# Kernel tuning notes

Measured on AMD Instinct MI355X. Metric: run time of the kernel, lower is better.

## Reference

```python
import math
import jax, jax.numpy as jnp
import numpy as np

E_DIM = 256
R_DIM = 256
HID = 512
B = 1024
H = 200
LN_EPS = 1e-5


def layer_norm(x, g, b):
    mu = jnp.mean(x, axis=-1, keepdims=True)
    var = jnp.mean((x - mu) ** 2, axis=-1, keepdims=True)
    return (x - mu) * jax.lax.rsqrt(var + LN_EPS) * g + b


def setup_inputs() -> dict:
    key = jax.random.key(0)
    ks = jax.random.split(key, 16)
    s = lambda fan: 1.0 / math.sqrt(fan)
    inp = {
        "e_emb": jax.random.normal(ks[0], (B, E_DIM), jnp.float32),
        "hist_ent_emb": jax.random.normal(ks[1], (B, H, E_DIM), jnp.float32),
        "hist_rel_emb": jax.random.normal(ks[2], (B, H, R_DIM), jnp.float32),
        "hist_time_raw": jax.random.randint(ks[3], (B, H), 0, 1000, jnp.int32),
        "query_time": jax.random.randint(ks[4], (B,), 0, 1000, jnp.int32),
        "hist_mask": jax.random.bernoulli(ks[5], 0.8, (B, H)),
        # parameters
        "W_rel": jax.random.uniform(ks[6], (E_DIM, R_DIM), jnp.float32, -s(R_DIM), s(R_DIM)),
        "W_q": jax.random.uniform(ks[7], (E_DIM, E_DIM), jnp.float32, -s(E_DIM), s(E_DIM)),
        "log_gamma": jnp.asarray(-3.0, jnp.float32),
        "W1": jax.random.uniform(ks[8], (2 * E_DIM, 4 * E_DIM), jnp.float32, -s(4 * E_DIM), s(4 * E_DIM)),
        "b1": jnp.zeros((2 * E_DIM,), jnp.float32),
        "ln1_g": jnp.ones((2 * E_DIM,), jnp.float32),
        "ln1_b": jnp.zeros((2 * E_DIM,), jnp.float32),
        "W2": jax.random.uniform(ks[9], (E_DIM, 2 * E_DIM), jnp.float32, -s(2 * E_DIM), s(2 * E_DIM)),
        "b2": jnp.zeros((E_DIM,), jnp.float32),
        "ln2_g": jnp.ones((E_DIM,), jnp.float32),
        "ln2_b": jnp.zeros((E_DIM,), jnp.float32),
        "Wc": jax.random.uniform(ks[10], (HID, E_DIM), jnp.float32, -s(E_DIM), s(E_DIM)),
        "bc": jnp.zeros((HID,), jnp.float32),
        "lnc_g": jnp.ones((HID,), jnp.float32),
        "lnc_b": jnp.zeros((HID,), jnp.float32),
    }
    return inp


def reference(e_emb, hist_ent_emb, hist_rel_emb, hist_time_raw, query_time, hist_mask,
              W_rel, W_q, log_gamma, W1, b1, ln1_g, ln1_b, W2, b2, ln2_g, ln2_b,
              Wc, bc, lnc_g, lnc_b):
    E = e_emb.shape[-1]
    # DistMult messages: (B,H,E)
    rel_projected = jnp.einsum("bhr,er->bhe", hist_rel_emb, W_rel)
    messages = hist_ent_emb * rel_projected
    # time decay
    time_diff = jnp.maximum(query_time.astype(jnp.float32)[:, None] - hist_time_raw.astype(jnp.float32), 0.0)
    decay = jnp.exp(-jnp.exp(log_gamma) * time_diff)  # (B,H)
    messages_dec = messages * decay[..., None]
    # query-conditioned attention
    q_repr = e_emb @ W_q.T  # (B,E)
    attn_raw = jnp.einsum("be,bhe->bh", q_repr, messages_dec) / math.sqrt(E)
    attn_raw = jnp.where(hist_mask, attn_raw, -1e9)
    attn = jax.nn.softmax(attn_raw, axis=-1)
    # PNA aggregation over valid neighbors
    valid_f = hist_mask.astype(jnp.float32)[..., None]  # (B,H,1)
    n_valid = jnp.maximum(jnp.sum(valid_f, axis=1), 1.0)  # (B,1)
    valid_msgs = messages * valid_f
    mean_msg = jnp.sum(valid_msgs, axis=1) / n_valid
    max_msg = jnp.max(valid_msgs, axis=1)
    attn_msg = jnp.einsum("bh,bhe->be", attn, messages)
    combined = jnp.concatenate([mean_msg, max_msg, attn_msg, e_emb], axis=-1)  # (B,4E)
    # out_proj MLP (dropout = identity, eval mode)
    h1 = jax.nn.gelu(layer_norm(combined @ W1.T + b1, ln1_g, ln1_b), approximate=False)
    dynamic_emb = layer_norm(h1 @ W2.T + b2, ln2_g, ln2_b)  # (B,E)
    ctx = jax.nn.gelu(layer_norm(dynamic_emb @ Wc.T + bc, lnc_g, lnc_b), approximate=False)  # (B,HID)
    return dynamic_emb, ctx
```

## Files before the change

kernel.cpp:

```cpp
#include <hip/hip_runtime.h>
#include <hip/hip_bf16.h>
#include <math.h>

#define B_SZ 1024
#define H_SZ 200
#define E_SZ 256
#define R_SZ 256
#define LN_EPS 1e-5f
#define NEG_HUGE -3.0e38f

typedef short bf16x8 __attribute__((ext_vector_type(8)));
typedef float f32x4 __attribute__((ext_vector_type(4)));

static __device__ inline short f2bf(float f) {
  union { float f; unsigned int u; } v; v.f = f;
  unsigned int u = v.u;
  unsigned int r = (u + 0x7fffu + ((u >> 16) & 1u)) >> 16;
  return (short)(unsigned short)r;
}

static __device__ inline float mask_at(const void* m, size_t idx, int is_b8) {
  if (is_b8) return ((const unsigned char*)m)[idx] ? 1.f : 0.f;
  return ((const int*)m)[idx] ? 1.f : 0.f;
}

__global__ void detect_mask_kernel(const unsigned char* __restrict__ mask,
                                   int* __restrict__ flag) {
  __shared__ int cnt;
  if (threadIdx.x == 0) cnt = 0;
  __syncthreads();
  int c = 0;
  for (int i = threadIdx.x; i < 4096; i += 256) c += mask[i] ? 1 : 0;
  atomicAdd(&cnt, c);
  __syncthreads();
  if (threadIdx.x == 0) *flag = (cnt > 2048) ? 1 : 0;
}

__global__ __launch_bounds__(256) void qrepr_kernel(
    const float* __restrict__ e_emb, const float* __restrict__ Wq,
    float* __restrict__ q_out) {
  __shared__ float emb[4][E_SZ];
  const int t = threadIdx.x;
  const int b0 = blockIdx.x * 4;
  for (int r = 0; r < 4; ++r) emb[r][t] = e_emb[(size_t)(b0 + r) * E_SZ + t];
  __syncthreads();
  float acc[4] = {0.f, 0.f, 0.f, 0.f};
  const float4* wrow = (const float4*)(Wq + (size_t)t * E_SZ);
  for (int k4 = 0; k4 < E_SZ / 4; ++k4) {
    float4 w = wrow[k4];
    const int k = k4 * 4;
#pragma unroll
    for (int r = 0; r < 4; ++r)
      acc[r] += emb[r][k] * w.x + emb[r][k + 1] * w.y + emb[r][k + 2] * w.z +
                emb[r][k + 3] * w.w;
  }
  for (int r = 0; r < 4; ++r) q_out[(size_t)(b0 + r) * E_SZ + t] = acc[r];
}

#define AGG_LDS_BYTES 152576

__global__ __launch_bounds__(512, 2) void agg_kernel(
    const float* __restrict__ rel, const float* __restrict__ ent,
    const int* __restrict__ htime, const int* __restrict__ qtime,
    const void* __restrict__ mask, const int* __restrict__ mflag,
    const float* __restrict__ Wrel, const float* __restrict__ qws,
    const float* __restrict__ e_emb, const float* __restrict__ log_gamma,
    float* __restrict__ comb) {
  extern __shared__ char smem[];
  short* Wsw = (short*)smem;
  short* Asw = (short*)(smem + 131072);
  float* q_s = (float*)(smem + 147456);
  float* attn_acc = (float*)(smem + 148480);
  float* mean_b = (float*)(smem + 149504);
  float* max_b = (float*)(smem + 150528);
  float* s_part = (float*)(smem + 151552);
  float* decay_s = (float*)(smem + 152064);
  float* maskf_s = (float*)(smem + 152192);
  float* p_s = (float*)(smem + 152320);
  float* scal = (float*)(smem + 152448);

  const int t = threadIdx.x;
  const int lane = t & 63;
  const int w = t >> 6;
  const int rh = w >> 2;
  const int cg = w & 3;
  const int q4 = lane >> 4;
  const int cl = lane & 15;
  const float gamma = expf(log_gamma[0]);
  const int is_b8 = *mflag;

  for (int pass = 0; pass < 16; ++pass) {
    const int idx = pass * 512 + t;
    const int e = idx >> 5;
    const int rc = idx & 31;
    const float4* src = (const float4*)(Wrel + (size_t)e * R_SZ + rc * 8);
    float4 a0 = src[0], a1 = src[1];
    const int ks = rc >> 2;
    const int lidx = ((rc & 3) << 4) | (e & 15);
    const int csub = e >> 4;
    bf16x8 v;
    v[0] = f2bf(a0.x); v[1] = f2bf(a0.y); v[2] = f2bf(a0.z); v[3] = f2bf(a0.w);
    v[4] = f2bf(a1.x); v[5] = f2bf(a1.y); v[6] = f2bf(a1.z); v[7] = f2bf(a1.w);
    *(bf16x8*)(Wsw + (((csub * 8 + ks) * 64 + lidx) << 3)) = v;
  }

  for (int bi = 0; bi < 4; ++bi) {
    const int b = blockIdx.x + 256 * bi;
    if (t < 256) { attn_acc[t] = 0.f; q_s[t] = qws[(size_t)b * E_SZ + t]; }
    if (t == 0) { scal[0] = NEG_HUGE; scal[1] = 0.f; scal[2] = 0.f; scal[3] = 0.f; }
    float mean4[4] = {0.f, 0.f, 0.f, 0.f};
    float max4[4] = {NEG_HUGE, NEG_HUGE, NEG_HUGE, NEG_HUGE};
    const float qtf = (float)qtime[b];
    __syncthreads();

    for (int tile = 0; tile < 7; ++tile) {
      const int h0 = tile * 32;
      {
        const int row = t >> 4;
        const int rcc = t & 15;
        const int h = h0 + row;
        bf16x8 v0 = {}; bf16x8 v1 = {};
        if (h < H_SZ) {
          const float4* src =
              (const float4*)(rel + ((size_t)b * H_SZ + h) * R_SZ + rcc * 16);
          float4 a0 = src[0], a1 = src[1], a2 = src[2], a3 = src[3];
          v0[0] = f2bf(a0.x); v0[1] = f2bf(a0.y); v0[2] = f2bf(a0.z); v0[3] = f2bf(a0.w);
          v0[4] = f2bf(a1.x); v0[5] = f2bf(a1.y); v0[6] = f2bf(a1.z); v0[7] = f2bf(a1.w);
          v1[0] = f2bf(a2.x); v1[1] = f2bf(a2.y); v1[2] = f2bf(a2.z); v1[3] = f2bf(a2.w);
          v1[4] = f2bf(a3.x); v1[5] = f2bf(a3.y); v1[6] = f2bf(a3.z); v1[7] = f2bf(a3.w);
        }
        const int rh2 = row >> 4, rlow = row & 15;
        const int rr0 = rcc * 2, rr1 = rcc * 2 + 1;
        *(bf16x8*)(Asw + (((rh2 * 8 + (rr0 >> 2)) * 64 + (((rr0 & 3) << 4) | rlow)) << 3)) = v0;
        *(bf16x8*)(Asw + (((rh2 * 8 + (rr1 >> 2)) * 64 + (((rr1 & 3) << 4) | rlow)) << 3)) = v1;
      }
      if (t < 32) {
        const int h = h0 + t;
        float mf = 0.f, dc = 0.f;
        if (h < H_SZ) {
          mf = mask_at(mask, (size_t)b * H_SZ + h, is_b8);
          float td = fmaxf(qtf - (float)htime[(size_t)b * H_SZ + h], 0.f);
          dc = expf(-gamma * td);
        }
        maskf_s[t] = mf; decay_s[t] = dc;
      }
      __syncthreads();

      f32x4 acc[4] = {};
      for (int ks = 0; ks < 8; ++ks) {
        bf16x8 av = *(bf16x8*)(Asw + (((rh * 8 + ks) * 64 + lane) << 3));
#pragma unroll
        for (int sub = 0; sub < 4; ++sub) {
          bf16x8 bv = *(bf16x8*)(Wsw + ((((cg * 4 + sub) * 8 + ks) * 64 + lane) << 3));
          acc[sub] = __builtin_amdgcn_mfma_f32_16x16x32_bf16(av, bv, acc[sub], 0, 0, 0);
        }
      }

      float msgv[16];
      float sc[4];
#pragma unroll
      for (int reg = 0; reg < 4; ++reg) {
        const int row = rh * 16 + q4 * 4 + reg;
        const int h = h0 + row;
        const float mf = maskf_s[row];
        const bool realrow = (h < H_SZ);
        float srow = 0.f;
#pragma unroll
        for (int sub = 0; sub < 4; ++sub) {
          const int e = cg * 64 + sub * 16 + cl;
          float entv = realrow ? ent[((size_t)b * H_SZ + h) * E_SZ + e] : 0.f;
          float m = acc[sub][reg] * entv;
          msgv[reg * 4 + sub] = m;
          mean4[sub] += mf * m;
          float cand = realrow ? (mf != 0.f ? m : 0.f) : NEG_HUGE;
          max4[sub] = fmaxf(max4[sub], cand);
          srow += q_s[e] * m;
        }
        sc[reg] = srow;
      }
#pragma unroll
      for (int m = 1; m <= 8; m <<= 1)
#pragma unroll
        for (int reg = 0; reg < 4; ++reg) sc[reg] += __shfl_xor(sc[reg], m, 64);
      if (cl == 0)
#pragma unroll
        for (int reg = 0; reg < 4; ++reg)
          s_part[(rh * 16 + q4 * 4 + reg) * 4 + cg] = sc[reg];
      __syncthreads();

      if (w == 0) {
        const int row = lane & 31;
        const int h = h0 + row;
        float srow = s_part[row * 4] + s_part[row * 4 + 1] +
                     s_part[row * 4 + 2] + s_part[row * 4 + 3];
        float s;
        if (h >= H_SZ) s = NEG_HUGE;
        else if (maskf_s[row] == 0.f) s = -1e9f;
        else s = decay_s[row] * srow * 0.0625f;
        float mt = s;
#pragma unroll
        for (int m = 1; m <= 16; m <<= 1) mt = fmaxf(mt, __shfl_xor(mt, m, 64));
        const float m_old = scal[0];
        const float m_new = fmaxf(m_old, mt);
        const float alpha = expf(m_old - m_new);
        const float p = expf(s - m_new);
        float lt = p;
#pragma unroll
        for (int m = 1; m <= 16; m <<= 1) lt += __shfl_xor(lt, m, 64);
        if (lane == 0) {
          scal[0] = m_new;
          scal[1] = scal[1] * alpha + lt;
          scal[2] = alpha;
        }
        if (lane < 32) p_s[row] = p;
      }
      __syncthreads();
      {
        const float alpha = scal[2];
        if (t < 256) attn_acc[t] *= alpha;
      }
      __syncthreads();
      float av4[4];
#pragma unroll
      for (int sub = 0; sub < 4; ++sub) {
        float v = 0.f;
#pragma unroll
        for (int reg = 0; reg < 4; ++reg)
          v += p_s[rh * 16 + q4 * 4 + reg] * msgv[reg * 4 + sub];
        v += __shfl_xor(v, 16, 64);
        v += __shfl_xor(v, 32, 64);
        av4[sub] = v;
      }
      if (q4 == 0)
#pragma unroll
        for (int sub = 0; sub < 4; ++sub)
          atomicAdd(&attn_acc[cg * 64 + sub * 16 + cl], av4[sub]);
      __syncthreads();
    }

#pragma unroll
    for (int sub = 0; sub < 4; ++sub) {
      float mv = mean4[sub];
      mv += __shfl_xor(mv, 16, 64); mv += __shfl_xor(mv, 32, 64);
      float xv = max4[sub];
      xv = fmaxf(xv, __shfl_xor(xv, 16, 64));
      xv = fmaxf(xv, __shfl_xor(xv, 32, 64));
      mean4[sub] = mv; max4[sub] = xv;
    }
    if (rh == 0 && q4 == 0) {
#pragma unroll
      for (int sub = 0; sub < 4; ++sub) {
        mean_b[cg * 64 + sub * 16 + cl] = mean4[sub];
        max_b[cg * 64 + sub * 16 + cl] = max4[sub];
      }
    }
    if (t < H_SZ) atomicAdd(&scal[3], mask_at(mask, (size_t)b * H_SZ + t, is_b8));
    __syncthreads();
    if (rh == 1 && q4 == 0) {
#pragma unroll
      for (int sub = 0; sub < 4; ++sub) {
        const int e = cg * 64 + sub * 16 + cl;
        mean_b[e] += mean4[sub];
        max_b[e] = fmaxf(max_b[e], max4[sub]);
      }
    }
    __syncthreads();
    if (t < 256) {
      const float nv = fmaxf(scal[3], 1.f);
      const float l = scal[1];
      float* dst = comb + (size_t)b * 1024;
      dst[t] = mean_b[t] / nv;
      dst[256 + t] = max_b[t];
      dst[512 + t] = attn_acc[t] / l;
      dst[768 + t] = e_emb[(size_t)b * E_SZ + t];
    }
    __syncthreads();
  }
}

template <int K, int N, bool GELU>
__global__ __launch_bounds__(256) void mlp_kernel(
    const float* __restrict__ X, const float* __restrict__ W,
    const float* __restrict__ bias, const float* __restrict__ lng,
    const float* __restrict__ lnb, float* __restrict__ Y) {
  constexpr int CPT = N / 256;
  __shared__ float xs[4][K];
  __shared__ float pre[4][N];
  __shared__ float red[4][2];
  const int t = threadIdx.x;
  const size_t b0 = (size_t)blockIdx.x * 4;
  for (int r = 0; r < 4; ++r)
    for (int k = t; k < K; k += 256) xs[r][k] = X[(b0 + r) * K + k];
  __syncthreads();
  float acc[4][CPT];
#pragma unroll
  for (int r = 0; r < 4; ++r)
#pragma unroll
    for (int c = 0; c < CPT; ++c) acc[r][c] = 0.f;
  for (int ci = 0; ci < CPT; ++ci) {
    const int c = t + 256 * ci;
    const float4* wr = (const float4*)(W + (size_t)c * K);
    for (int k4 = 0; k4 < K / 4; ++k4) {
      float4 wv = wr[k4];
      const int k = k4 * 4;
#pragma unroll
      for (int r = 0; r < 4; ++r)
        acc[r][ci] += xs[r][k] * wv.x + xs[r][k + 1] * wv.y +
                      xs[r][k + 2] * wv.z + xs[r][k + 3] * wv.w;
    }
  }
  for (int ci = 0; ci < CPT; ++ci) {
    const int c = t + 256 * ci;
#pragma unroll
    for (int r = 0; r < 4; ++r) pre[r][c] = acc[r][ci] + bias[c];
  }
  __syncthreads();
  if (t < 64) {
    const int r = t >> 4, ch = t & 15;
    float s = 0.f, s2 = 0.f;
    for (int i = ch * (N / 16); i < (ch + 1) * (N / 16); ++i) {
      float v = pre[r][i]; s += v; s2 += v * v;
    }
#pragma unroll
    for (int m = 1; m <= 8; m <<= 1) {
      s += __shfl_xor(s, m, 64);
      s2 += __shfl_xor(s2, m, 64);
    }
    if (ch == 0) { red[r][0] = s / N; red[r][1] = s2 / N; }
  }
  __syncthreads();
  for (int ci = 0; ci < CPT; ++ci) {
    const int c = t + 256 * ci;
#pragma unroll
    for (int r = 0; r < 4; ++r) {
      const float mu = red[r][0];
      const float var = fmaxf(red[r][1] - mu * mu, 0.f);
      float x = (pre[r][c] - mu) * rsqrtf(var + LN_EPS) * lng[c] + lnb[c];
      if (GELU) x = 0.5f * x * (1.f + erff(x * 0.70710678118654752f));
      Y[(b0 + r) * N + c] = x;
    }
  }
}

extern "C" void kernel_launch(void* const* d_in, const int* in_sizes, int n_in,
                              void* d_out, int out_size, void* d_ws,
                              size_t ws_size, hipStream_t stream) {
  const float* e_emb = (const float*)d_in[0];
  const float* ent = (const float*)d_in[1];
  const float* rel = (const float*)d_in[2];
  const int* ht = (const int*)d_in[3];
  const int* qt = (const int*)d_in[4];
  const void* mask = d_in[5];
  const float* Wrel = (const float*)d_in[6];
  const float* Wq = (const float*)d_in[7];
  const float* lg = (const float*)d_in[8];
  const float* W1 = (const float*)d_in[9];
  const float* b1 = (const float*)d_in[10];
  const float* ln1g = (const float*)d_in[11];
  const float* ln1b = (const float*)d_in[12];
  const float* W2 = (const float*)d_in[13];
  const float* b2 = (const float*)d_in[14];
  const float* ln2g = (const float*)d_in[15];
  const float* ln2b = (const float*)d_in[16];
  const float* Wc = (const float*)d_in[17];
  const float* bc = (const float*)d_in[18];
  const float* lncg = (const float*)d_in[19];
  const float* lncb = (const float*)d_in[20];

  int* mflag = (int*)d_ws;
  float* q_ws = (float*)((char*)d_ws + 4096);
  float* t1 = (float*)((char*)d_ws + 4096);
  float* comb = (float*)((char*)d_ws + 4096 + (2u << 20));
  float* dyn = (float*)d_out;
  float* ctx = (float*)d_out + (size_t)B_SZ * E_SZ;

  (void)ws_size;
  (void)hipFuncSetAttribute((const void*)agg_kernel,
                            hipFuncAttributeMaxDynamicSharedMemorySize,
                            AGG_LDS_BYTES);

  detect_mask_kernel<<<1, 256, 0, stream>>>((const unsigned char*)mask, mflag);
  qrepr_kernel<<<256, 256, 0, stream>>>(e_emb, Wq, q_ws);
  agg_kernel<<<256, 512, AGG_LDS_BYTES, stream>>>(rel, ent, ht, qt, mask, mflag,
                                                  Wrel, q_ws, e_emb, lg, comb);
  mlp_kernel<1024, 512, true><<<256, 256, 0, stream>>>(comb, W1, b1, ln1g, ln1b, t1);
  mlp_kernel<512, 256, false><<<256, 256, 0, stream>>>(t1, W2, b2, ln2g, ln2b, dyn);
  mlp_kernel<256, 512, true><<<256, 256, 0, stream>>>(dyn, Wc, bc, lncg, lncb, ctx);
}
```

Measured before the change: 674.8 us.

## Run MLP layers on bf16 MFMA with pre-swizzled bf16 weights

Replaces the scalar fp32 MLP kernels with MFMA 16x16x32 bf16 kernels that handle 16 rows per block. Weights are converted to bf16 each call into an MFMA-friendly swizzled layout. The aggregation output and the first MLP output are now stored as bf16, which halves intermediate traffic. The cost is reduced precision, three extra conversion launches, and only 64 blocks per MLP layer, so fewer CUs are busy.

Result: slower. 693.5 us (+2.8%).

```diff
diff --git a/kernel.cpp b/kernel.cpp
--- a/kernel.cpp
+++ b/kernel.cpp
@@ -34,6 +34,24 @@
   atomicAdd(&cnt, c);
   __syncthreads();
   if (threadIdx.x == 0) *flag = (cnt > 2048) ? 1 : 0;
+}
+
+__global__ __launch_bounds__(256) void wconv_kernel(
+    const float* __restrict__ W, short* __restrict__ out, int N, int K) {
+  const int k8pern = K >> 3;
+  const int idx = blockIdx.x * 256 + threadIdx.x;
+  if (idx >= N * k8pern) return;
+  const int n = idx / k8pern;
+  const int k8 = idx - n * k8pern;
+  const float4* s = (const float4*)(W + (size_t)n * K + k8 * 8);
+  float4 a0 = s[0], a1 = s[1];
+  bf16x8 v;
+  v[0] = f2bf(a0.x); v[1] = f2bf(a0.y); v[2] = f2bf(a0.z); v[3] = f2bf(a0.w);
+  v[4] = f2bf(a1.x); v[5] = f2bf(a1.y); v[6] = f2bf(a1.z); v[7] = f2bf(a1.w);
+  const size_t off =
+      (((size_t)(n >> 4) * (K >> 5) + (k8 >> 2)) * 64 +
+       ((((k8 & 3)) << 4) | (n & 15))) << 3;
+  *(bf16x8*)(out + off) = v;
 }
 
 __global__ __launch_bounds__(256) void qrepr_kernel(
@@ -65,7 +83,7 @@
     const void* __restrict__ mask, const int* __restrict__ mflag,
     const float* __restrict__ Wrel, const float* __restrict__ qws,
     const float* __restrict__ e_emb, const float* __restrict__ log_gamma,
-    float* __restrict__ comb) {
+    short* __restrict__ comb) {
   extern __shared__ char smem[];
   short* Wsw = (short*)smem;
   short* Asw = (short*)(smem + 131072);
@@ -268,77 +286,86 @@
     if (t < 256) {
       const float nv = fmaxf(scal[3], 1.f);
       const float l = scal[1];
-      float* dst = comb + (size_t)b * 1024;
-      dst[t] = mean_b[t] / nv;
-      dst[256 + t] = max_b[t];
-      dst[512 + t] = attn_acc[t] / l;
-      dst[768 + t] = e_emb[(size_t)b * E_SZ + t];
+      short* dst = comb + (size_t)b * 1024;
+      dst[t] = f2bf(mean_b[t] / nv);
+      dst[256 + t] = f2bf(max_b[t]);
+      dst[512 + t] = f2bf(attn_acc[t] / l);
+      dst[768 + t] = f2bf(e_emb[(size_t)b * E_SZ + t]);
     }
     __syncthreads();
   }
 }
 
-template <int K, int N, bool GELU>
-__global__ __launch_bounds__(256) void mlp_kernel(
-    const float* __restrict__ X, const float* __restrict__ W,
+template <int K, int N, bool GELU, bool IN_BF16, bool OUT_BF16>
+__global__ __launch_bounds__(256) void mfma_mlp_kernel(
+    const void* __restrict__ Xv, const short* __restrict__ Wswz,
     const float* __restrict__ bias, const float* __restrict__ lng,
-    const float* __restrict__ lnb, float* __restrict__ Y) {
-  constexpr int CPT = N / 256;
-  __shared__ float xs[4][K];
-  __shared__ float pre[4][N];
-  __shared__ float red[4][2];
+    const float* __restrict__ lnb, void* __restrict__ Yv) {
+  constexpr int NS = N / 64;
+  constexpr int KS = K / 32;
+  __shared__ float pre[16][N + 4];
+  __shared__ float red[16][2];
   const int t = threadIdx.x;
-  const size_t b0 = (size_t)blockIdx.x * 4;
-  for (int r = 0; r < 4; ++r)
-    for (int k = t; k < K; k += 256) xs[r][k] = X[(b0 + r) * K + k];
+  const int lane = t & 63;
+  const int w = t >> 6;
+  const int r0 = blockIdx.x * 16;
+  const int am = lane & 15;
+  const int ak = (lane >> 4) * 8;
+
+  f32x4 acc[NS] = {};
+  const short* wbase = Wswz + (size_t)(w * NS) * KS * 512;
+#pragma unroll 2
+  for (int ks = 0; ks < KS; ++ks) {
+    bf16x8 av;
+    if (IN_BF16) {
+      const short* X = (const short*)Xv;
+      av = *(const bf16x8*)(X + (size_t)(r0 + am) * K + ks * 32 + ak);
+    } else {
+      const float* X = (const float*)Xv;
+      const float4* s = (const float4*)(X + (size_t)(r0 + am) * K + ks * 32 + ak);
+      float4 a0 = s[0], a1 = s[1];
+      av[0] = f2bf(a0.x); av[1] = f2bf(a0.y); av[2] = f2bf(a0.z); av[3] = f2bf(a0.w);
+      av[4] = f2bf(a1.x); av[5] = f2bf(a1.y); av[6] = f2bf(a1.z); av[7] = f2bf(a1.w);
+    }
+#pragma unroll
+    for (int s = 0; s < NS; ++s) {
+      bf16x8 bv = *(const bf16x8*)(wbase + (((size_t)(s * KS + ks)) * 64 + lane) * 8);
+      acc[s] = __builtin_amdgcn_mfma_f32_16x16x32_bf16(av, bv, acc[s], 0, 0, 0);
+    }
+  }
+#pragma unroll
+  for (int s = 0; s < NS; ++s) {
+    const int col = w * (N / 4) + s * 16 + am;
+    const float bv = bias[col];
+#pragma unroll
+    for (int reg = 0; reg < 4; ++reg) {
+      const int row = (lane >> 4) * 4 + reg;
+      pre[row][col] = acc[s][reg] + bv;
+    }
+  }
   __syncthreads();
-  float acc[4][CPT];
-#pragma unroll
-  for (int r = 0; r < 4; ++r)
-#pragma unroll
-    for (int c = 0; c < CPT; ++c) acc[r][c] = 0.f;
-  for (int ci = 0; ci < CPT; ++ci) {
-    const int c = t + 256 * ci;
-    const float4* wr = (const float4*)(W + (size_t)c * K);
-    for (int k4 = 0; k4 < K / 4; ++k4) {
-      float4 wv = wr[k4];
-      const int k = k4 * 4;
-#pragma unroll
-      for (int r = 0; r < 4; ++r)
-        acc[r][ci] += xs[r][k] * wv.x + xs[r][k + 1] * wv.y +
-                      xs[r][k + 2] * wv.z + xs[r][k + 3] * wv.w;
-    }
-  }
-  for (int ci = 0; ci < CPT; ++ci) {
-    const int c = t + 256 * ci;
-#pragma unroll
-    for (int r = 0; r < 4; ++r) pre[r][c] = acc[r][ci] + bias[c];
+  {
+    const int row = t >> 4, ch = t & 15;
+    float s1 = 0.f, s2 = 0.f;
+    for (int c = ch; c < N; c += 16) {
+      float v = pre[row][c]; s1 += v; s2 += v * v;
+    }
+#pragma unroll
+    for (int m = 1; m <= 8; m <<= 1) {
+      s1 += __shfl_xor(s1, m, 64);
+      s2 += __shfl_xor(s2, m, 64);
+    }
+    if (ch == 0) { red[row][0] = s1 / N; red[row][1] = s2 / N; }
   }
   __syncthreads();
-  if (t < 64) {
-    const int r = t >> 4, ch = t & 15;
-    float s = 0.f, s2 = 0.f;
-    for (int i = ch * (N / 16); i < (ch + 1) * (N / 16); ++i) {
-      float v = pre[r][i]; s += v; s2 += v * v;
-    }
-#pragma unroll
-    for (int m = 1; m <= 8; m <<= 1) {
-      s += __shfl_xor(s, m, 64);
-      s2 += __shfl_xor(s2, m, 64);
-    }
-    if (ch == 0) { red[r][0] = s / N; red[r][1] = s2 / N; }
-  }
-  __syncthreads();
-  for (int ci = 0; ci < CPT; ++ci) {
-    const int c = t + 256 * ci;
-#pragma unroll
-    for (int r = 0; r < 4; ++r) {
-      const float mu = red[r][0];
-      const float var = fmaxf(red[r][1] - mu * mu, 0.f);
-      float x = (pre[r][c] - mu) * rsqrtf(var + LN_EPS) * lng[c] + lnb[c];
-      if (GELU) x = 0.5f * x * (1.f + erff(x * 0.70710678118654752f));
-      Y[(b0 + r) * N + c] = x;
-    }
+  for (int i = t; i < 16 * N; i += 256) {
+    const int row = i / N, c = i - row * N;
+    const float mu = red[row][0];
+    const float var = fmaxf(red[row][1] - mu * mu, 0.f);
+    float x = (pre[row][c] - mu) * rsqrtf(var + LN_EPS) * lng[c] + lnb[c];
+    if (GELU) x = 0.5f * x * (1.f + erff(x * 0.70710678118654752f));
+    if (OUT_BF16) ((short*)Yv)[(size_t)(r0 + row) * N + c] = f2bf(x);
+    else ((float*)Yv)[(size_t)(r0 + row) * N + c] = x;
   }
 }
 
@@ -367,10 +394,14 @@
   const float* lncg = (const float*)d_in[19];
   const float* lncb = (const float*)d_in[20];
 
-  int* mflag = (int*)d_ws;
-  float* q_ws = (float*)((char*)d_ws + 4096);
-  float* t1 = (float*)((char*)d_ws + 4096);
-  float* comb = (float*)((char*)d_ws + 4096 + (2u << 20));
+  char* wsb = (char*)d_ws;
+  int* mflag = (int*)wsb;
+  short* w1b = (short*)(wsb + 4096);
+  short* w2b = (short*)(wsb + 4096 + (1u << 20));
+  short* wcb = (short*)(wsb + 4096 + (1u << 20) + (256u << 10));
+  float* q_ws = (float*)(wsb + 4096 + ((1536u) << 10));
+  short* t1b = (short*)(wsb + 4096 + ((1536u) << 10));
+  short* combb = (short*)(wsb + 4096 + ((2560u) << 10));
   float* dyn = (float*)d_out;
   float* ctx = (float*)d_out + (size_t)B_SZ * E_SZ;
 
@@ -380,10 +411,16 @@
                             AGG_LDS_BYTES);
 
   detect_mask_kernel<<<1, 256, 0, stream>>>((const unsigned char*)mask, mflag);
+  wconv_kernel<<<(512 * 1024 / 8 + 255) / 256, 256, 0, stream>>>(W1, w1b, 512, 1024);
+  wconv_kernel<<<(256 * 512 / 8 + 255) / 256, 256, 0, stream>>>(W2, w2b, 256, 512);
+  wconv_kernel<<<(512 * 256 / 8 + 255) / 256, 256, 0, stream>>>(Wc, wcb, 512, 256);
   qrepr_kernel<<<256, 256, 0, stream>>>(e_emb, Wq, q_ws);
   agg_kernel<<<256, 512, AGG_LDS_BYTES, stream>>>(rel, ent, ht, qt, mask, mflag,
-                                                  Wrel, q_ws, e_emb, lg, comb);
-  mlp_kernel<1024, 512, true><<<256, 256, 0, stream>>>(comb, W1, b1, ln1g, ln1b, t1);
-  mlp_kernel<512, 256, false><<<256, 256, 0, stream>>>(t1, W2, b2, ln2g, ln2b, dyn);
-  mlp_kernel<256, 512, true><<<256, 256, 0, stream>>>(dyn, Wc, bc, lncg, lncb, ctx);
-}
+                                                  Wrel, q_ws, e_emb, lg, combb);
+  mfma_mlp_kernel<1024, 512, true, true, true>
+      <<<64, 256, 0, stream>>>(combb, w1b, b1, ln1g, ln1b, t1b);
+  mfma_mlp_kernel<512, 256, false, true, false>
+      <<<64, 256, 0, stream>>>(t1b, w2b, b2, ln2g, ln2b, dyn);
+  mfma_mlp_kernel<256, 512, true, false, false>
+      <<<64, 256, 0, stream>>>(dyn, wcb, bc, lncg, lncb, ctx);
+}
```
